# Kernel optimization log

Hardware: AMD Instinct MI355X
Metric: run time of the kernel (lower is better)

Reference implementation:

```python
import jax, jax.numpy as jnp
import numpy as np

N = 12          # microphones
K = 512         # GCC window length (lags)
RES_T = 32      # theta resolution
RES_P = 64      # phi resolution
FS = 16000.0    # sampling frequency
C = 343.0       # speed of sound
B, T = 8, 32    # batch, frames
EPS = 1e-12


def _mic_positions():
    # 5 cm radius uniform circular array in the xy-plane (matches rn init arg)
    ang = 2.0 * np.pi * np.arange(N) / N
    return np.stack([0.05 * np.cos(ang), 0.05 * np.sin(ang), np.zeros(N)], axis=1)


def _compute_tau0():
    """Precompute integer lag indices tau0[n, m, theta, phi] exactly as the torch
    module does (nearest lag on the circular GCC axis), vectorized."""
    theta = np.linspace(0.0, np.pi / 2, RES_T)
    phi = np.linspace(-np.pi, np.pi, RES_P + 1)[:-1]
    # unit direction vectors r: [RES_T, RES_P, 3]
    r = np.stack([np.outer(np.sin(theta), np.cos(phi)),
                  np.outer(np.sin(theta), np.sin(phi)),
                  np.tile(np.cos(theta)[:, None], [1, RES_P])], axis=2)
    rn = _mic_positions()
    diff = rn[None, :, :] - rn[:, None, :]            # [k, l, 3] = rn[l] - rn[k]
    imtdf = np.einsum('tpc,klc->tpkl', r, diff) / C   # TDOA in seconds
    # nearest lag; ceil(x - 0.5) reproduces np.argmin tie-breaking on the
    # tau grid [0..K/2, -K/2+1..-1] (ties go to floor for >0, more-negative for <0)
    lag = np.ceil(imtdf * FS - 0.5).astype(np.int64)
    lag = np.clip(lag, -(K // 2) + 1, K // 2)
    tau0 = lag.transpose(2, 3, 0, 1)                  # [N, N, RES_T, RES_P]
    tau0 = np.where(tau0 < 0, tau0 + K, tau0)         # wrap negative lags (circular GCC)
    return jnp.asarray(tau0, dtype=jnp.int32)


def setup_inputs() -> dict:
    key = jax.random.key(0)
    x = jax.random.normal(key, (B, T, N, N, K), dtype=jnp.float32)
    return {"x": x, "tau0": _compute_tau0()}


def reference(x, tau0):
    # x: [..., N, N, K], tau0: [N, N, RES_T, RES_P]
    lead = x.shape[:-3]
    x2 = x.reshape(lead + (N * N, K))                       # [..., P2, K]
    idx = tau0.reshape(N * N, RES_T * RES_P)                # [P2, G]
    idx_b = jnp.broadcast_to(idx, lead + idx.shape)
    g = jnp.take_along_axis(x2, idx_b, axis=-1)             # [..., P2, G]
    maps = g.sum(axis=-2).reshape(lead + (RES_T, RES_P))    # accumulate over mic pairs
    # normalize: zero-mean over the map, then divide by max (original adds eps first)
    maps = maps - jnp.mean(maps, axis=(-1, -2), keepdims=True) + EPS
    maps = maps / jnp.max(maps, axis=(-1, -2), keepdims=True)
    return maps
```

## Files before the change

kernel.cpp:

```cpp
#include <hip/hip_runtime.h>

#define NPAIR  144
#define KLEN   512
#define GPTS   2048
#define NFRM   256
#define FPB    4
#define NFG    (NFRM / FPB)
#define GSPLIT 4
#define GPB    (GPTS / GSPLIT)
#define NSLOT  16
#define NJ4    (NPAIR / 4)
#define EPSV   1e-12f

__global__ __launch_bounds__(512)
void srp_gather_kernel(const float* __restrict__ x,
                       const int* __restrict__ tau0,
                       float* __restrict__ maps) {
    __shared__ __align__(16) float xc[NPAIR * NSLOT * FPB];

    const int bi = blockIdx.x;
    const int fg = bi & (NFG - 1);
    const int gs = bi >> 6;
    const int t  = threadIdx.x;
    const int g  = gs * GPB + t;

    for (int i = t; i < NPAIR * FPB * 2; i += 512) {
        int pair = i >> 3;
        int fr   = (i >> 1) & 3;
        int seg  = i & 1;
        const float* src = x + ((size_t)(fg * FPB + fr) * NPAIR + pair) * KLEN
                             + (seg ? 504 : 0);
        int base = pair * NSLOT + seg * 8;
        #pragma unroll
        for (int jj = 0; jj < 2; ++jj) {
            float4 v = ((const float4*)src)[jj];
            xc[(base + jj * 4 + 0) * FPB + fr] = v.x;
            xc[(base + jj * 4 + 1) * FPB + fr] = v.y;
            xc[(base + jj * 4 + 2) * FPB + fr] = v.z;
            xc[(base + jj * 4 + 3) * FPB + fr] = v.w;
        }
    }

    unsigned dj[NJ4];
    #pragma unroll
    for (int j4 = 0; j4 < NJ4; ++j4) {
        unsigned d = 0;
        #pragma unroll
        for (int b = 0; b < 4; ++b) {
            int v = tau0[(j4 * 4 + b) * GPTS + g];
            d |= (((unsigned)v & 15u) << 4) << (8 * b);
        }
        dj[j4] = d;
    }

    __syncthreads();

    const char* xb = (const char*)xc;
    float4 acc = {0.f, 0.f, 0.f, 0.f};
    #pragma unroll
    for (int j4 = 0; j4 < NJ4; ++j4) {
        unsigned d = dj[j4];
        #pragma unroll
        for (int b = 0; b < 4; ++b) {
            unsigned off = (d >> (8 * b)) & 0xf0u;
            const float4 v = *(const float4*)(xb + (((j4 * 4 + b) << 8) + off));
            acc.x += v.x; acc.y += v.y; acc.z += v.z; acc.w += v.w;
        }
    }

    float* mp = maps + (size_t)(fg * FPB) * GPTS + g;
    mp[0 * GPTS] = acc.x;
    mp[1 * GPTS] = acc.y;
    mp[2 * GPTS] = acc.z;
    mp[3 * GPTS] = acc.w;
}

__global__ __launch_bounds__(256)
void srp_norm_kernel(const float* __restrict__ maps, float* __restrict__ out) {
    __shared__ float red[5];
    const int f = blockIdx.x;
    const int t = threadIdx.x;
    const float4* p = (const float4*)(maps + (size_t)f * GPTS);
    float4 s0 = p[t], s1 = p[t + 256];

    const int wave = t >> 6, lane = t & 63;

    float sm = s0.x + s0.y + s0.z + s0.w + s1.x + s1.y + s1.z + s1.w;
    #pragma unroll
    for (int off = 32; off > 0; off >>= 1) sm += __shfl_down(sm, off, 64);
    if (lane == 0) red[wave] = sm;
    __syncthreads();
    if (t == 0) red[4] = (red[0] + red[1] + red[2] + red[3]) * (1.0f / (float)GPTS);
    __syncthreads();
    const float mean = red[4];

    s0.x = s0.x - mean + EPSV; s0.y = s0.y - mean + EPSV;
    s0.z = s0.z - mean + EPSV; s0.w = s0.w - mean + EPSV;
    s1.x = s1.x - mean + EPSV; s1.y = s1.y - mean + EPSV;
    s1.z = s1.z - mean + EPSV; s1.w = s1.w - mean + EPSV;

    float mx = fmaxf(fmaxf(fmaxf(s0.x, s0.y), fmaxf(s0.z, s0.w)),
                     fmaxf(fmaxf(s1.x, s1.y), fmaxf(s1.z, s1.w)));
    #pragma unroll
    for (int off = 32; off > 0; off >>= 1) mx = fmaxf(mx, __shfl_down(mx, off, 64));
    __syncthreads();
    if (lane == 0) red[wave] = mx;
    __syncthreads();
    if (t == 0) red[4] = fmaxf(fmaxf(red[0], red[1]), fmaxf(red[2], red[3]));
    __syncthreads();
    const float inv = 1.0f / red[4];

    float4* o = (float4*)(out + (size_t)f * GPTS);
    o[t]       = make_float4(s0.x * inv, s0.y * inv, s0.z * inv, s0.w * inv);
    o[t + 256] = make_float4(s1.x * inv, s1.y * inv, s1.z * inv, s1.w * inv);
}

extern "C" void kernel_launch(void* const* d_in, const int* in_sizes, int n_in,
                              void* d_out, int out_size, void* d_ws, size_t ws_size,
                              hipStream_t stream) {
    const float* x    = (const float*)d_in[0];
    const int*   tau0 = (const int*)d_in[1];
    float* out = (float*)d_out;

    float* maps = (float*)d_ws;

    srp_gather_kernel<<<NFG * GSPLIT, 512, 0, stream>>>(x, tau0, maps);
    srp_norm_kernel<<<NFRM, 256, 0, stream>>>(maps, out);
}
```

Baseline: 108.4 us.

## Fuse gather and normalization into one cooperative kernel with grid sync

Merges the gather and normalization kernels into a single cooperative launch. Each block reduces per-frame sum and max of its partial map slice into a small partials buffer, then a grid-wide sync lets every block finish the frame statistics and write normalized output directly. This drops the intermediate maps round-trip through global memory and the second launch. In exchange it adds a grid barrier and cooperative-launch overhead. It also uses the identity max(x - mean + eps) = max(x) - mean + eps.

```diff
diff --git a/kernel.cpp b/kernel.cpp
--- a/kernel.cpp
+++ b/kernel.cpp
@@ -1,4 +1,7 @@
 #include <hip/hip_runtime.h>
+#include <hip/hip_cooperative_groups.h>
+
+namespace cg = cooperative_groups;
 
 #define NPAIR  144
 #define KLEN   512
@@ -13,10 +16,14 @@
 #define EPSV   1e-12f
 
 __global__ __launch_bounds__(512)
-void srp_gather_kernel(const float* __restrict__ x,
-                       const int* __restrict__ tau0,
-                       float* __restrict__ maps) {
+void srp_fused_kernel(const float* __restrict__ x,
+                      const int* __restrict__ tau0,
+                      float2* __restrict__ partials,
+                      float* __restrict__ out) {
     __shared__ __align__(16) float xc[NPAIR * NSLOT * FPB];
+    __shared__ float redS[8 * FPB];
+    __shared__ float redX[8 * FPB];
+    __shared__ float2 nrm[FPB];
 
     const int bi = blockIdx.x;
     const int fg = bi & (NFG - 1);
@@ -68,51 +75,56 @@
         }
     }
 
-    float* mp = maps + (size_t)(fg * FPB) * GPTS + g;
-    mp[0 * GPTS] = acc.x;
-    mp[1 * GPTS] = acc.y;
-    mp[2 * GPTS] = acc.z;
-    mp[3 * GPTS] = acc.w;
-}
+    float4 sm = acc, mx = acc;
+    #pragma unroll
+    for (int off = 32; off > 0; off >>= 1) {
+        sm.x += __shfl_down(sm.x, off, 64);
+        sm.y += __shfl_down(sm.y, off, 64);
+        sm.z += __shfl_down(sm.z, off, 64);
+        sm.w += __shfl_down(sm.w, off, 64);
+        mx.x = fmaxf(mx.x, __shfl_down(mx.x, off, 64));
+        mx.y = fmaxf(mx.y, __shfl_down(mx.y, off, 64));
+        mx.z = fmaxf(mx.z, __shfl_down(mx.z, off, 64));
+        mx.w = fmaxf(mx.w, __shfl_down(mx.w, off, 64));
+    }
+    const int wave = t >> 6, lane = t & 63;
+    if (lane == 0) {
+        redS[wave * 4 + 0] = sm.x; redS[wave * 4 + 1] = sm.y;
+        redS[wave * 4 + 2] = sm.z; redS[wave * 4 + 3] = sm.w;
+        redX[wave * 4 + 0] = mx.x; redX[wave * 4 + 1] = mx.y;
+        redX[wave * 4 + 2] = mx.z; redX[wave * 4 + 3] = mx.w;
+    }
+    __syncthreads();
+    if (t < FPB) {
+        float S = 0.f, X = -3.402823466e38f;
+        #pragma unroll
+        for (int w = 0; w < 8; ++w) {
+            S += redS[w * 4 + t];
+            X = fmaxf(X, redX[w * 4 + t]);
+        }
+        partials[(fg * FPB + t) * GSPLIT + gs] = make_float2(S, X);
+    }
+    __threadfence();
+    cg::this_grid().sync();
 
-__global__ __launch_bounds__(256)
-void srp_norm_kernel(const float* __restrict__ maps, float* __restrict__ out) {
-    __shared__ float red[5];
-    const int f = blockIdx.x;
-    const int t = threadIdx.x;
-    const float4* p = (const float4*)(maps + (size_t)f * GPTS);
-    float4 s0 = p[t], s1 = p[t + 256];
+    if (t < FPB) {
+        float S = 0.f, X = -3.402823466e38f;
+        #pragma unroll
+        for (int k = 0; k < GSPLIT; ++k) {
+            float2 p = partials[(fg * FPB + t) * GSPLIT + k];
+            S += p.x;
+            X = fmaxf(X, p.y);
+        }
+        float mean = S * (1.0f / (float)GPTS);
+        nrm[t] = make_float2(mean, 1.0f / ((X - mean) + EPSV));
+    }
+    __syncthreads();
 
-    const int wave = t >> 6, lane = t & 63;
-
-    float sm = s0.x + s0.y + s0.z + s0.w + s1.x + s1.y + s1.z + s1.w;
-    #pragma unroll
-    for (int off = 32; off > 0; off >>= 1) sm += __shfl_down(sm, off, 64);
-    if (lane == 0) red[wave] = sm;
-    __syncthreads();
-    if (t == 0) red[4] = (red[0] + red[1] + red[2] + red[3]) * (1.0f / (float)GPTS);
-    __syncthreads();
-    const float mean = red[4];
-
-    s0.x = s0.x - mean + EPSV; s0.y = s0.y - mean + EPSV;
-    s0.z = s0.z - mean + EPSV; s0.w = s0.w - mean + EPSV;
-    s1.x = s1.x - mean + EPSV; s1.y = s1.y - mean + EPSV;
-    s1.z = s1.z - mean + EPSV; s1.w = s1.w - mean + EPSV;
-
-    float mx = fmaxf(fmaxf(fmaxf(s0.x, s0.y), fmaxf(s0.z, s0.w)),
-                     fmaxf(fmaxf(s1.x, s1.y), fmaxf(s1.z, s1.w)));
-    #pragma unroll
-    for (int off = 32; off > 0; off >>= 1) mx = fmaxf(mx, __shfl_down(mx, off, 64));
-    __syncthreads();
-    if (lane == 0) red[wave] = mx;
-    __syncthreads();
-    if (t == 0) red[4] = fmaxf(fmaxf(red[0], red[1]), fmaxf(red[2], red[3]));
-    __syncthreads();
-    const float inv = 1.0f / red[4];
-
-    float4* o = (float4*)(out + (size_t)f * GPTS);
-    o[t]       = make_float4(s0.x * inv, s0.y * inv, s0.z * inv, s0.w * inv);
-    o[t + 256] = make_float4(s1.x * inv, s1.y * inv, s1.z * inv, s1.w * inv);
+    float* op = out + (size_t)(fg * FPB) * GPTS + g;
+    op[0 * GPTS] = ((acc.x - nrm[0].x) + EPSV) * nrm[0].y;
+    op[1 * GPTS] = ((acc.y - nrm[1].x) + EPSV) * nrm[1].y;
+    op[2 * GPTS] = ((acc.z - nrm[2].x) + EPSV) * nrm[2].y;
+    op[3 * GPTS] = ((acc.w - nrm[3].x) + EPSV) * nrm[3].y;
 }
 
 extern "C" void kernel_launch(void* const* d_in, const int* in_sizes, int n_in,
@@ -121,9 +133,10 @@
     const float* x    = (const float*)d_in[0];
     const int*   tau0 = (const int*)d_in[1];
     float* out = (float*)d_out;
+    float2* partials = (float2*)d_ws;
 
-    float* maps = (float*)d_ws;
-
-    srp_gather_kernel<<<NFG * GSPLIT, 512, 0, stream>>>(x, tau0, maps);
-    srp_norm_kernel<<<NFRM, 256, 0, stream>>>(maps, out);
+    void* args[] = { (void*)&x, (void*)&tau0, (void*)&partials, (void*)&out };
+    hipLaunchCooperativeKernel((void*)srp_fused_kernel,
+                               dim3(NFG * GSPLIT), dim3(512),
+                               args, 0, stream);
 }
```

Measured after the change: 172.6 us. 1.59x slower.
